# Optimization experiments

Hardware: AMD Instinct MI355X
Metric: run time of the kernel (lower is better)

Reference implementation:

```python
import jax, jax.numpy as jnp
import numpy as np

OUT, IN, GROUP = 11008, 4096, 64
NUM_GROUPS = IN // GROUP  # pad = 0 since IN % GROUP == 0


def setup_inputs() -> dict:
    key = jax.random.key(0)
    k_x, k_q, k_s, k_b = jax.random.split(key, 4)
    x = jax.random.normal(k_x, (4, 2048, IN), dtype=jnp.float32)
    # int4 symmetric codes in [-8, 7], stored as int8 like the torch buffer
    qweight = jax.random.randint(k_q, (OUT, NUM_GROUPS, GROUP), -8, 8).astype(jnp.int8)
    # positive per-group scales (amax/7 in the original), stored fp16
    scales = (jax.random.uniform(k_s, (OUT, NUM_GROUPS), dtype=jnp.float32) * 0.02 + 1e-3).astype(jnp.float16)
    bias = (jax.random.normal(k_b, (OUT,), dtype=jnp.float32) * 0.02).astype(jnp.float16)
    return {"x": x, "qweight": qweight, "scales": scales, "bias": bias}


def reference(x, qweight, scales, bias):
    # Fused dequant: w[o, g*GROUP + j] = q[o, g, j] * scales[o, g]
    w = (qweight.astype(jnp.float16) * scales[:, :, None]).reshape(OUT, IN)
    w = w.astype(x.dtype)  # original casts dequantized weight to x.dtype
    # F.linear(x, w, bias): y = x @ w.T + b  -> [B, S, OUT]
    return jnp.einsum('bsi,oi->bso', x, w) + bias.astype(x.dtype)
```

## Files before the change

kernel.cpp:

```cpp
#include <hip/hip_runtime.h>
#include <hip/hip_fp16.h>
#include <stdint.h>


#define M_DIM 8192
#define N_DIM 11008
#define K_DIM 4096
#define MT_TILES 32
#define NT_TILES 43
#define K_TILES 128
#define SLAB 8192

typedef short short8 __attribute__((ext_vector_type(8)));
typedef float floatx4 __attribute__((ext_vector_type(4)));

__device__ __forceinline__ unsigned short f2bf(float f) {
  union { float f; uint32_t u; } c; c.f = f;
  uint32_t u = c.u;
  return (unsigned short)((u + 0x7FFFu + ((u >> 16) & 1u)) >> 16);
}

__device__ __forceinline__ float load_sc(const void* p, size_t idx, bool is_f32) {
  if (is_f32) return ((const float*)p)[idx];
  return __half2float(((const __half*)p)[idx]);
}

__device__ __forceinline__ bool sniff_q_is_i32(const void* qv) {
  const int* w = (const int*)qv;
  bool ok = true;
  #pragma unroll
  for (int j = 0; j < 16; ++j) {
    int v = w[j];
    ok = ok && (v == (int)(signed char)(v & 0xFF));
  }
  return ok;
}
__device__ __forceinline__ bool sniff_s_is_f32(const void* sv) {
  const float* f = (const float*)sv;
  bool ok = true;
  #pragma unroll
  for (int j = 0; j < 8; ++j) {
    float v = f[j];
    ok = ok && (v > 4e-4f) && (v < 6e-2f);
  }
  return ok;
}

__device__ __forceinline__ void gload_lds16(const short* g, short* l) {
  __builtin_amdgcn_global_load_lds(
      (const __attribute__((address_space(1))) uint32_t*)g,
      (__attribute__((address_space(3))) uint32_t*)l, 16, 0, 0);
}

__global__ __launch_bounds__(256)
void cvt_x_pack(const float* __restrict__ x, short* __restrict__ xh) {
  const int b = blockIdx.x;
  const int mt = b >> 8;
  const int rem = b & 255;
  const int kt = rem >> 1, half = rem & 1;
  const int tid = threadIdx.x;
  const int r = half * 128 + (tid >> 1);
  const int s0 = (tid & 1) * 2;
  const int k0 = kt * 32 + s0 * 8;

  const float4* p = (const float4*)(x + (size_t)(mt * 256 + r) * K_DIM + k0);
  float4 f0 = p[0], f1 = p[1], f2 = p[2], f3 = p[3];
  short8 h0, h1;
  h0[0]=f2bf(f0.x); h0[1]=f2bf(f0.y); h0[2]=f2bf(f0.z); h0[3]=f2bf(f0.w);
  h0[4]=f2bf(f1.x); h0[5]=f2bf(f1.y); h0[6]=f2bf(f1.z); h0[7]=f2bf(f1.w);
  h1[0]=f2bf(f2.x); h1[1]=f2bf(f2.y); h1[2]=f2bf(f2.z); h1[3]=f2bf(f2.w);
  h1[4]=f2bf(f3.x); h1[5]=f2bf(f3.y); h1[6]=f2bf(f3.z); h1[7]=f2bf(f3.w);

  const int w = (r >> 1) & 3;
  short* slab = xh + ((size_t)mt * K_TILES + kt) * SLAB;
  *(short8*)&slab[r * 32 + ((s0    ) ^ w) * 8] = h0;
  *(short8*)&slab[r * 32 + ((s0 + 1) ^ w) * 8] = h1;
}

__global__ __launch_bounds__(256)
void deq_w_pack(const void* __restrict__ qv, const void* __restrict__ sv,
                short* __restrict__ wq) {
  const bool q_is_i32 = sniff_q_is_i32(qv);
  const bool s_is_f32 = sniff_s_is_f32(sv);
  const int b = blockIdx.x;
  const int nt = b >> 8;
  const int rem = b & 255;
  const int kt = rem >> 1, half = rem & 1;
  const int tid = threadIdx.x;
  const int r = half * 128 + (tid >> 1);
  const int s0 = (tid & 1) * 2;
  const int o = nt * 256 + r;
  const int k0 = kt * 32 + s0 * 8;

  const float s = load_sc(sv, (size_t)o * 64 + (kt >> 1), s_is_f32);

  int codes[16];
  if (q_is_i32) {
    const int* qq = (const int*)qv + (size_t)o * K_DIM + k0;
    #pragma unroll
    for (int j = 0; j < 4; ++j) {
      int4 t = ((const int4*)qq)[j];
      codes[j*4+0]=t.x; codes[j*4+1]=t.y; codes[j*4+2]=t.z; codes[j*4+3]=t.w;
    }
  } else {
    union { int4 v; int8_t c[16]; } u;
    u.v = *(const int4*)((const int8_t*)qv + (size_t)o * K_DIM + k0);
    #pragma unroll
    for (int j = 0; j < 16; ++j) codes[j] = (int)u.c[j];
  }

  short8 h0, h1;
  #pragma unroll
  for (int j = 0; j < 8; ++j) h0[j] = f2bf((float)codes[j] * s);
  #pragma unroll
  for (int j = 0; j < 8; ++j) h1[j] = f2bf((float)codes[8 + j] * s);

  const int w = (r >> 1) & 3;
  short* slab = wq + ((size_t)nt * K_TILES + kt) * SLAB;
  *(short8*)&slab[r * 32 + ((s0    ) ^ w) * 8] = h0;
  *(short8*)&slab[r * 32 + ((s0 + 1) ^ w) * 8] = h1;
}

__global__ __launch_bounds__(512)
void gemm8(const short* __restrict__ xh, const short* __restrict__ wq,
           const void* __restrict__ sv, const void* __restrict__ bv,
           float* __restrict__ C) {
  __shared__ __align__(16) short lds[4 * 2 * SLAB];

  const bool s_is_f32 = sniff_s_is_f32(sv);

  const int tid  = threadIdx.x;
  const int lane = tid & 63;
  const int wid  = tid >> 6;
  const int wm = wid >> 2, wn = wid & 3;
  const int lr = lane & 15, lk = lane >> 4;

  const int bid = blockIdx.x;
  const int xcd = bid & 7;
  const int seq = bid >> 3;
  const int nt  = seq >> 2;
  const int mt  = xcd * 4 + (seq & 3);

  const short* Aslab = xh + (size_t)mt * K_TILES * SLAB;
  const short* Bslab = wq + (size_t)nt * K_TILES * SLAB;

  const int swz8 = (lk ^ ((lr >> 1) & 3)) << 3;
  int aoff[8], boff[4];
  #pragma unroll
  for (int mi = 0; mi < 8; ++mi) aoff[mi] = (wm * 128 + mi * 16 + lr) * 32 + swz8;
  #pragma unroll
  for (int ni = 0; ni < 4; ++ni) boff[ni] = (wn * 64 + ni * 16 + lr) * 32 + swz8;

  floatx4 acc[8][4];
  #pragma unroll
  for (int i = 0; i < 8; ++i)
    #pragma unroll
    for (int j = 0; j < 4; ++j)
      acc[i][j] = (floatx4){0.f, 0.f, 0.f, 0.f};

  short8 fa[8], fb[4], ga[8], gb[4];

#define STAGE(t) do {                                                   \
    const short* gA_ = Aslab + (size_t)(t) * SLAB;                      \
    const short* gB_ = Bslab + (size_t)(t) * SLAB;                      \
    short* lA_ = &lds[((t) & 3) * (2 * SLAB)];                          \
    short* lB_ = lA_ + SLAB;                                            \
    gload_lds16(gA_ + tid * 8,        lA_ + tid * 8);                   \
    gload_lds16(gA_ + 4096 + tid * 8, lA_ + 4096 + tid * 8);            \
    gload_lds16(gB_ + tid * 8,        lB_ + tid * 8);                   \
    gload_lds16(gB_ + 4096 + tid * 8, lB_ + 4096 + tid * 8);            \
  } while (0)

#define LOADF(da, db, t) do {                                           \
    const short* lA_ = &lds[((t) & 3) * (2 * SLAB)];                    \
    const short* lB_ = lA_ + SLAB;                                      \
    _Pragma("unroll")                                                   \
    for (int mi = 0; mi < 8; ++mi) da[mi] = *(const short8*)&lA_[aoff[mi]]; \
    _Pragma("unroll")                                                   \
    for (int ni = 0; ni < 4; ++ni) db[ni] = *(const short8*)&lB_[boff[ni]]; \
  } while (0)

#define DOMFMA(sa, sb) do {                                             \
    __builtin_amdgcn_s_setprio(1);                                      \
    _Pragma("unroll")                                                   \
    for (int mi = 0; mi < 8; ++mi)                                      \
      _Pragma("unroll")                                                 \
      for (int ni = 0; ni < 4; ++ni)                                    \
        acc[mi][ni] = __builtin_amdgcn_mfma_f32_16x16x32_bf16(          \
            sa[mi], sb[ni], acc[mi][ni], 0, 0, 0);                      \
    __builtin_amdgcn_s_setprio(0);                                      \
  } while (0)

#define FENCE asm volatile("" ::: "memory")
#define VMCNT(n) asm volatile("s_waitcnt vmcnt(" #n ")" ::: "memory")
#define BARRIER do { FENCE; __builtin_amdgcn_s_barrier(); FENCE; } while (0)

  STAGE(0); STAGE(1); STAGE(2);
  VMCNT(8);
  BARRIER;
  LOADF(fa, fb, 0);

  for (int kt = 0; kt < 124; kt += 2) {
    VMCNT(4);
    BARRIER;
    STAGE(kt + 3);
    LOADF(ga, gb, kt + 1);
    DOMFMA(fa, fb);
    VMCNT(4);
    BARRIER;
    STAGE(kt + 4);
    LOADF(fa, fb, kt + 2);
    DOMFMA(ga, gb);
  }

  VMCNT(4);
  BARRIER;
  STAGE(127);
  LOADF(ga, gb, 125);
  DOMFMA(fa, fb);
  VMCNT(4);
  BARRIER;
  LOADF(fa, fb, 126);
  DOMFMA(ga, gb);
  VMCNT(0);
  BARRIER;
  LOADF(ga, gb, 127);
  DOMFMA(fa, fb);
  DOMFMA(ga, gb);

#undef STAGE
#undef LOADF
#undef DOMFMA
#undef FENCE
#undef VMCNT
#undef BARRIER

  #pragma unroll
  for (int ni = 0; ni < 4; ++ni) {
    const int col = nt * 256 + wn * 64 + ni * 16 + lr;
    const float bvf = load_sc(bv, (size_t)col, s_is_f32);
    #pragma unroll
    for (int mi = 0; mi < 8; ++mi) {
      const int rbase = mt * 256 + wm * 128 + mi * 16 + lk * 4;
      #pragma unroll
      for (int rr = 0; rr < 4; ++rr)
        C[(size_t)(rbase + rr) * N_DIM + col] = acc[mi][ni][rr] + bvf;
    }
  }
}

__global__ __launch_bounds__(256)
void gemm_fused(const float* __restrict__ x, const void* __restrict__ qv,
                const void* __restrict__ sv, const void* __restrict__ bv,
                float* __restrict__ C) {
  __shared__ __align__(16) short As[128 * 64];
  __shared__ __align__(16) short Bs[128 * 64];

  const bool q_is_i32 = sniff_q_is_i32(qv);
  const bool s_is_f32 = sniff_s_is_f32(sv);

  const int tid  = threadIdx.x;
  const int lane = tid & 63;
  const int wid  = tid >> 6;
  const int wm = wid >> 1, wn = wid & 1;
  const int lr = lane & 15, lk = lane >> 4;

  const int nwg = gridDim.x;
  const int cpx = nwg >> 3;
  const int bid = blockIdx.x;
  const int swz = (bid & 7) * cpx + (bid >> 3);
  const int per_g = 4 * 86;
  const int g = swz / per_g;
  const int r = swz - g * per_g;
  const int mt = (g << 2) + (r & 3);
  const int nt = r >> 2;

  const int row0 = mt * 128;
  const int col0 = nt * 128;

  floatx4 acc[4][4];
  #pragma unroll
  for (int i = 0; i < 4; ++i)
    #pragma unroll
    for (int j = 0; j < 4; ++j)
      acc[i][j] = (floatx4){0.f, 0.f, 0.f, 0.f};

  for (int kt = 0; kt < K_DIM / 64; ++kt) {
    const int k0 = kt * 64;
    #pragma unroll
    for (int i = 0; i < 4; ++i) {
      const int cid = i * 256 + tid;
      const int arow = cid >> 3, ac = (cid & 7) << 3;
      const float4* p = (const float4*)(x + (size_t)(row0 + arow) * K_DIM + k0 + ac);
      float4 a = p[0], b = p[1];
      short8 h;
      h[0]=f2bf(a.x); h[1]=f2bf(a.y); h[2]=f2bf(a.z); h[3]=f2bf(a.w);
      h[4]=f2bf(b.x); h[5]=f2bf(b.y); h[6]=f2bf(b.z); h[7]=f2bf(b.w);
      *(short8*)&As[arow * 64 + ac] = h;
    }
    #pragma unroll
    for (int i = 0; i < 2; ++i) {
      const int cid = i * 256 + tid;
      const int brow = cid >> 2, bc = (cid & 3) << 4;
      const float s = load_sc(sv, (size_t)(col0 + brow) * 64 + kt, s_is_f32);
      int codes[16];
      if (q_is_i32) {
        const int* qq = (const int*)qv + (size_t)(col0 + brow) * K_DIM + k0 + bc;
        #pragma unroll
        for (int j = 0; j < 4; ++j) {
          int4 t = ((const int4*)qq)[j];
          codes[j*4+0]=t.x; codes[j*4+1]=t.y; codes[j*4+2]=t.z; codes[j*4+3]=t.w;
        }
      } else {
        union { int4 v; int8_t c[16]; } u;
        u.v = *(const int4*)((const int8_t*)qv + (size_t)(col0 + brow) * K_DIM + k0 + bc);
        #pragma unroll
        for (int j = 0; j < 16; ++j) codes[j] = (int)u.c[j];
      }
      short8 h0, h1;
      #pragma unroll
      for (int j = 0; j < 8; ++j) h0[j] = f2bf((float)codes[j] * s);
      #pragma unroll
      for (int j = 0; j < 8; ++j) h1[j] = f2bf((float)codes[8 + j] * s);
      *(short8*)&Bs[brow * 64 + bc]     = h0;
      *(short8*)&Bs[brow * 64 + bc + 8] = h1;
    }
    __syncthreads();
    #pragma unroll
    for (int ks = 0; ks < 2; ++ks) {
      short8 a[4], b[4];
      #pragma unroll
      for (int mi = 0; mi < 4; ++mi)
        a[mi] = *(const short8*)&As[(wm * 64 + mi * 16 + lr) * 64 + ks * 32 + lk * 8];
      #pragma unroll
      for (int ni = 0; ni < 4; ++ni)
        b[ni] = *(const short8*)&Bs[(wn * 64 + ni * 16 + lr) * 64 + ks * 32 + lk * 8];
      #pragma unroll
      for (int mi = 0; mi < 4; ++mi)
        #pragma unroll
        for (int ni = 0; ni < 4; ++ni)
          acc[mi][ni] = __builtin_amdgcn_mfma_f32_16x16x32_bf16(
              a[mi], b[ni], acc[mi][ni], 0, 0, 0);
    }
    __syncthreads();
  }

  #pragma unroll
  for (int ni = 0; ni < 4; ++ni) {
    const int col = col0 + wn * 64 + ni * 16 + lr;
    const float bvf = load_sc(bv, (size_t)col, s_is_f32);
    #pragma unroll
    for (int mi = 0; mi < 4; ++mi) {
      const int rbase = row0 + wm * 64 + mi * 16 + lk * 4;
      #pragma unroll
      for (int rr = 0; rr < 4; ++rr)
        C[(size_t)(rbase + rr) * N_DIM + col] = acc[mi][ni][rr] + bvf;
    }
  }
}

extern "C" void kernel_launch(void* const* d_in, const int* in_sizes, int n_in,
                              void* d_out, int out_size, void* d_ws, size_t ws_size,
                              hipStream_t stream) {
  const float* x  = (const float*)d_in[0];
  const void*  q  = (const void*)d_in[1];
  const void*  sc = (const void*)d_in[2];
  const void*  bs = (const void*)d_in[3];
  float* y = (float*)d_out;
  (void)in_sizes; (void)n_in; (void)out_size;

  const size_t xh_bytes = (size_t)M_DIM * K_DIM * 2;
  const size_t wq_bytes = (size_t)N_DIM * K_DIM * 2;

  if (ws_size >= xh_bytes + wq_bytes) {
    short* xh = (short*)d_ws;
    short* wq = (short*)((char*)d_ws + xh_bytes);
    cvt_x_pack<<<MT_TILES * 256, dim3(256), 0, stream>>>(x, xh);
    deq_w_pack<<<NT_TILES * 256, dim3(256), 0, stream>>>(q, sc, wq);
    gemm8<<<MT_TILES * NT_TILES, dim3(512), 0, stream>>>(xh, wq, sc, bs, y);
  } else {
    gemm_fused<<<(M_DIM / 128) * (N_DIM / 128), dim3(256), 0, stream>>>(x, q, sc, bs, y);
  }
}
```

Before: 761.8 us.

## Load B operand directly from global into registers in MFMA fragment layout

The dequant prep kernel now writes the weight tiles in a fragment-major layout, so each lane can read its MFMA B fragments straight from global memory with contiguous 16-byte loads. The GEMM stops staging B through LDS and keeps only the A tiles there, which halves shared memory use and removes the B LDS writes and reads. B fragments are double-buffered in registers and prefetched one k-tile ahead, with the vmcnt waits adjusted for the extra outstanding loads. The cost is that the B loads are now redundant across the two wm waves and exposed to global latency, and register pressure rises.

Result: slower. 855.2 us (+12.3%).

```diff
diff --git a/kernel.cpp b/kernel.cpp
--- a/kernel.cpp
+++ b/kernel.cpp
@@ -115,17 +115,17 @@
   #pragma unroll
   for (int j = 0; j < 8; ++j) h1[j] = f2bf((float)codes[8 + j] * s);
 
-  const int w = (r >> 1) & 3;
   short* slab = wq + ((size_t)nt * K_TILES + kt) * SLAB;
-  *(short8*)&slab[r * 32 + ((s0    ) ^ w) * 8] = h0;
-  *(short8*)&slab[r * 32 + ((s0 + 1) ^ w) * 8] = h1;
+  const int cb = r >> 4, lr = r & 15;
+  *(short8*)&slab[cb * 512 + (lr + 16 * (s0    )) * 8] = h0;
+  *(short8*)&slab[cb * 512 + (lr + 16 * (s0 + 1)) * 8] = h1;
 }
 
 __global__ __launch_bounds__(512)
 void gemm8(const short* __restrict__ xh, const short* __restrict__ wq,
            const void* __restrict__ sv, const void* __restrict__ bv,
            float* __restrict__ C) {
-  __shared__ __align__(16) short lds[4 * 2 * SLAB];
+  __shared__ __align__(16) short lds[4 * SLAB];
 
   const bool s_is_f32 = sniff_s_is_f32(sv);
 
@@ -145,11 +145,10 @@
   const short* Bslab = wq + (size_t)nt * K_TILES * SLAB;
 
   const int swz8 = (lk ^ ((lr >> 1) & 3)) << 3;
-  int aoff[8], boff[4];
+  int aoff[8];
   #pragma unroll
   for (int mi = 0; mi < 8; ++mi) aoff[mi] = (wm * 128 + mi * 16 + lr) * 32 + swz8;
-  #pragma unroll
-  for (int ni = 0; ni < 4; ++ni) boff[ni] = (wn * 64 + ni * 16 + lr) * 32 + swz8;
+  const int boff = (wn * 4) * 512 + lane * 8;
 
   floatx4 acc[8][4];
   #pragma unroll
@@ -158,26 +157,31 @@
     for (int j = 0; j < 4; ++j)
       acc[i][j] = (floatx4){0.f, 0.f, 0.f, 0.f};
 
-  short8 fa[8], fb[4], ga[8], gb[4];
-
-#define STAGE(t) do {                                                   \
+  short8 fa[8], ga[8], be[4], bo[4];
+
+#define FENCE asm volatile("" ::: "memory")
+#define VMCNT(n) asm volatile("s_waitcnt vmcnt(" #n ")" ::: "memory")
+#define BARRIER do { FENCE; __builtin_amdgcn_s_barrier(); FENCE; } while (0)
+
+#define STAGE_A(t) do {                                                 \
     const short* gA_ = Aslab + (size_t)(t) * SLAB;                      \
-    const short* gB_ = Bslab + (size_t)(t) * SLAB;                      \
-    short* lA_ = &lds[((t) & 3) * (2 * SLAB)];                          \
-    short* lB_ = lA_ + SLAB;                                            \
+    short* lA_ = &lds[((t) & 3) * SLAB];                                \
     gload_lds16(gA_ + tid * 8,        lA_ + tid * 8);                   \
     gload_lds16(gA_ + 4096 + tid * 8, lA_ + 4096 + tid * 8);            \
-    gload_lds16(gB_ + tid * 8,        lB_ + tid * 8);                   \
-    gload_lds16(gB_ + 4096 + tid * 8, lB_ + 4096 + tid * 8);            \
+    FENCE;                                                              \
   } while (0)
 
-#define LOADF(da, db, t) do {                                           \
-    const short* lA_ = &lds[((t) & 3) * (2 * SLAB)];                    \
-    const short* lB_ = lA_ + SLAB;                                      \
+#define LOADB(db, t) do {                                               \
+    const short* gB_ = Bslab + (size_t)(t) * SLAB + boff;               \
+    _Pragma("unroll")                                                   \
+    for (int ni = 0; ni < 4; ++ni) db[ni] = *(const short8*)(gB_ + ni * 512); \
+    FENCE;                                                              \
+  } while (0)
+
+#define LOADF_A(da, t) do {                                             \
+    const short* lA_ = &lds[((t) & 3) * SLAB];                          \
     _Pragma("unroll")                                                   \
     for (int mi = 0; mi < 8; ++mi) da[mi] = *(const short8*)&lA_[aoff[mi]]; \
-    _Pragma("unroll")                                                   \
-    for (int ni = 0; ni < 4; ++ni) db[ni] = *(const short8*)&lB_[boff[ni]]; \
   } while (0)
 
 #define DOMFMA(sa, sb) do {                                             \
@@ -191,45 +195,50 @@
     __builtin_amdgcn_s_setprio(0);                                      \
   } while (0)
 
-#define FENCE asm volatile("" ::: "memory")
-#define VMCNT(n) asm volatile("s_waitcnt vmcnt(" #n ")" ::: "memory")
-#define BARRIER do { FENCE; __builtin_amdgcn_s_barrier(); FENCE; } while (0)
-
-  STAGE(0); STAGE(1); STAGE(2);
+  STAGE_A(0);
+  STAGE_A(1);
+  LOADB(be, 0);
+  STAGE_A(2);
+  LOADB(bo, 1);
+  VMCNT(12);
+  BARRIER;
+  LOADF_A(fa, 0);
+
+  for (int kt = 0; kt < 124; kt += 2) {
+    VMCNT(10);
+    BARRIER;
+    STAGE_A(kt + 3);
+    LOADF_A(ga, kt + 1);
+    DOMFMA(fa, be);
+    LOADB(be, kt + 2);
+    VMCNT(10);
+    BARRIER;
+    STAGE_A(kt + 4);
+    LOADF_A(fa, kt + 2);
+    DOMFMA(ga, bo);
+    LOADB(bo, kt + 3);
+  }
+
+  VMCNT(10);
+  BARRIER;
+  STAGE_A(127);
+  LOADF_A(ga, 125);
+  DOMFMA(fa, be);
+  LOADB(be, 126);
+  VMCNT(10);
+  BARRIER;
+  LOADF_A(fa, 126);
+  DOMFMA(ga, bo);
+  LOADB(bo, 127);
   VMCNT(8);
   BARRIER;
-  LOADF(fa, fb, 0);
-
-  for (int kt = 0; kt < 124; kt += 2) {
-    VMCNT(4);
-    BARRIER;
-    STAGE(kt + 3);
-    LOADF(ga, gb, kt + 1);
-    DOMFMA(fa, fb);
-    VMCNT(4);
-    BARRIER;
-    STAGE(kt + 4);
-    LOADF(fa, fb, kt + 2);
-    DOMFMA(ga, gb);
-  }
-
-  VMCNT(4);
-  BARRIER;
-  STAGE(127);
-  LOADF(ga, gb, 125);
-  DOMFMA(fa, fb);
-  VMCNT(4);
-  BARRIER;
-  LOADF(fa, fb, 126);
-  DOMFMA(ga, gb);
-  VMCNT(0);
-  BARRIER;
-  LOADF(ga, gb, 127);
-  DOMFMA(fa, fb);
-  DOMFMA(ga, gb);
-
-#undef STAGE
-#undef LOADF
+  LOADF_A(ga, 127);
+  DOMFMA(fa, be);
+  DOMFMA(ga, bo);
+
+#undef STAGE_A
+#undef LOADB
+#undef LOADF_A
 #undef DOMFMA
 #undef FENCE
 #undef VMCNT
```
